# Performance work log

Hardware: AMD Instinct MI355X
Metric: run time of the kernel (lower is better)

Reference implementation:

```python
import jax, jax.numpy as jnp
import numpy as np

B = 1024          # batch
H = 512           # hidden_dim
T = 256           # seq_len
CD = 2            # coord_dim
LAT = 64 + 64 + 128  # total latent dim


def setup_inputs() -> dict:
    key = jax.random.key(0)
    ks = jax.random.split(key, 20)
    s = 0.05  # weight init scale
    rn = lambda k, shp: (jax.random.normal(k, shp, dtype=jnp.float32) * s)
    return {
        "z_primitive": jax.random.normal(ks[0], (B, 64), dtype=jnp.float32),
        "z_skill": jax.random.normal(ks[1], (B, 64), dtype=jnp.float32),
        "z_style": jax.random.normal(ks[2], (B, 128), dtype=jnp.float32),
        "W_proj": rn(ks[3], (2 * H, LAT)),
        "b_proj": jnp.zeros((2 * H,), jnp.float32),
        "Wih1": rn(ks[4], (4 * H, CD)),
        "Whh1": rn(ks[5], (4 * H, H)),
        "bih1": jnp.zeros((4 * H,), jnp.float32),
        "bhh1": jnp.zeros((4 * H,), jnp.float32),
        "Wih2": rn(ks[6], (4 * H, H)),
        "Whh2": rn(ks[7], (4 * H, H)),
        "bih2": jnp.zeros((4 * H,), jnp.float32),
        "bhh2": jnp.zeros((4 * H,), jnp.float32),
        "Wo1": rn(ks[8], (H // 2, H)),
        "bo1": jnp.zeros((H // 2,), jnp.float32),
        "Wo2": rn(ks[9], (CD, H // 2)),
        "bo2": jnp.zeros((CD,), jnp.float32),
    }


def _lstm_cell(x, h, c, Wih, Whh, bih, bhh):
    # PyTorch gate order: i, f, g, o
    gates = x @ Wih.T + h @ Whh.T + (bih + bhh)
    i, f, g, o = jnp.split(gates, 4, axis=1)
    c_new = jax.nn.sigmoid(f) * c + jax.nn.sigmoid(i) * jnp.tanh(g)
    h_new = jax.nn.sigmoid(o) * jnp.tanh(c_new)
    return h_new, c_new


def reference(z_primitive, z_skill, z_style, W_proj, b_proj,
              Wih1, Whh1, bih1, bhh1, Wih2, Whh2, bih2, bhh2,
              Wo1, bo1, Wo2, bo2):
    z = jnp.concatenate([z_primitive, z_skill, z_style], axis=1)  # [B, LAT]
    init = z @ W_proj.T + b_proj                                  # [B, 2H]
    h0 = init[:, :H]
    c0 = init[:, H:]
    x0 = jnp.zeros((z.shape[0], CD), init.dtype)

    def step(carry, _):
        x, h1, c1, h2, c2 = carry
        h1, c1 = _lstm_cell(x, h1, c1, Wih1, Whh1, bih1, bhh1)
        h2, c2 = _lstm_cell(h1, h2, c2, Wih2, Whh2, bih2, bhh2)
        # output MLP (Dropout inactive in eval)
        y = jax.nn.relu(h2 @ Wo1.T + bo1) @ Wo2.T + bo2  # [B, CD]
        return (y, h1, c1, h2, c2), y

    # h0/c0 repeated across both LSTM layers (repeat(2,1,1) in torch)
    _, ys = jax.lax.scan(step, (x0, h0, c0, h0, c0), None, length=T)
    return jnp.transpose(ys, (1, 0, 2))  # [B, T, CD]
```

## Files before the change

### kernel.cpp

```cpp
#include <hip/hip_runtime.h>
#include <math.h>

#define NB 1024
#define NH 512
#define NT 256
#define NCD 2

typedef unsigned short u16;
typedef __bf16 bf16x8 __attribute__((ext_vector_type(8)));
typedef float  f32x4  __attribute__((ext_vector_type(4)));

#define MFMA_BF16 __builtin_amdgcn_mfma_f32_16x16x32_bf16

__device__ __forceinline__ float sigf(float x) { return 1.0f / (1.0f + expf(-x)); }
__device__ __forceinline__ float b2f(u16 u) {
    union { unsigned i; float f; } v; v.i = ((unsigned)u) << 16; return v.f;
}
__device__ __forceinline__ u16 f2b(float f) {
    union { float f; unsigned i; } v; v.f = f;
    unsigned r = v.i + 0x7fffu + ((v.i >> 16) & 1u);
    return (u16)(r >> 16);
}

__device__ __forceinline__ void async_cp16(const void* gptr, void* lptr) {
    __builtin_amdgcn_global_load_lds(
        (const __attribute__((address_space(1))) unsigned int*)gptr,
        (__attribute__((address_space(3))) unsigned int*)lptr,
        16, 0, 0);
}

__global__ __launch_bounds__(256) void convert3(
    const float* __restrict__ a, const float* __restrict__ b,
    const float* __restrict__ c,
    u16* __restrict__ oa, u16* __restrict__ ob, u16* __restrict__ oc)
{
    const int i = blockIdx.x * 256 + threadIdx.x;
    oa[i] = f2b(a[i]); ob[i] = f2b(b[i]); oc[i] = f2b(c[i]);
}

__global__ __launch_bounds__(256) void convw1(
    const float* __restrict__ a, u16* __restrict__ o)
{
    const int i = blockIdx.x * 256 + threadIdx.x;
    o[i] = f2b(a[i]);
}

__global__ __launch_bounds__(256) void bsum_k(
    const float* __restrict__ bi1, const float* __restrict__ bh1,
    const float* __restrict__ bi2, const float* __restrict__ bh2,
    float* __restrict__ o1, float* __restrict__ o2)
{
    const int i = blockIdx.x * 256 + threadIdx.x;
    o1[i] = bi1[i] + bh1[i];
    o2[i] = bi2[i] + bh2[i];
}

__global__ __launch_bounds__(256) void init_kernel(
    const float* __restrict__ zp, const float* __restrict__ zs,
    const float* __restrict__ zst, const float* __restrict__ Wp,
    const float* __restrict__ bp,
    u16* __restrict__ h1, float* __restrict__ c1,
    u16* __restrict__ h2, float* __restrict__ c2)
{
    __shared__ float z[4][256];
    const int tid = threadIdx.x;
    const int b0  = blockIdx.x * 4;
    for (int i = tid; i < 4 * 256; i += 256) {
        const int bb = i >> 8, k = i & 255;
        float v;
        if (k < 64)       v = zp [(b0 + bb) * 64  + k];
        else if (k < 128) v = zs [(b0 + bb) * 64  + (k - 64)];
        else              v = zst[(b0 + bb) * 128 + (k - 128)];
        z[bb][k] = v;
    }
    __syncthreads();
    for (int rt = 0; rt < 4; ++rt) {
        const int r = rt * 256 + tid;
        const float bias = bp[r];
        float a0 = bias, a1 = bias, a2 = bias, a3 = bias;
        for (int k = 0; k < 256; ++k) {
            const float w = Wp[r * 256 + k];
            a0 += z[0][k] * w; a1 += z[1][k] * w;
            a2 += z[2][k] * w; a3 += z[3][k] * w;
        }
        const float acc[4] = {a0, a1, a2, a3};
        for (int bb = 0; bb < 4; ++bb) {
            const int b = b0 + bb;
            if (r < NH) {
                h1[b * NH + r] = f2b(acc[bb]);
                h2[b * NH + r] = f2b(acc[bb]);
            } else {
                c1[b * NH + r - NH] = acc[bb];
                c2[b * NH + r - NH] = acc[bb];
            }
        }
    }
}

__global__ __launch_bounds__(512, 4) void fused_out_lstm1(
    const u16* __restrict__ h2prev,
    const u16* __restrict__ A0,
    const u16* __restrict__ W0,
    const float* __restrict__ bsum,
    const float* __restrict__ Wx,
    const u16* __restrict__ W1b,
    const float* __restrict__ bo1, const float* __restrict__ Wo2,
    const float* __restrict__ bo2, float* __restrict__ outp,
    float* __restrict__ c, u16* __restrict__ hnext,
    const int t, const int do_lstm)
{
    __shared__ __align__(16) char smem[61440];
    float* eg  = (float*)smem;
    float* red = (float*)(smem + 36864);

    const int tid  = threadIdx.x;
    const int lane = tid & 63;
    const int wv   = tid >> 6;
    const int g    = wv & 3;
    const int mh   = wv >> 2;
    const int l15  = lane & 15;
    const int q    = lane >> 4;
    const int bx   = blockIdx.x;
    const int ut   = (bx & 7) * 2 + ((bx >> 3) & 1);
    const int grp  = bx >> 4;
    const int b0   = grp * 32;
    const int u0   = ut * 32;

    int goffW0, goffW1, goffA = 0, goffO[4];
    {
        const int c0 = (wv * 2) * 64 + lane;
        const int w0r = c0 >> 3;
        goffW0 = ((w0r >> 5) * NH + u0 + (w0r & 31)) * NH + (((c0 & 7) ^ (w0r & 7)) * 8);
        const int c1i = (wv * 2 + 1) * 64 + lane;
        const int w1r = c1i >> 3;
        goffW1 = ((w1r >> 5) * NH + u0 + (w1r & 31)) * NH + (((c1i & 7) ^ (w1r & 7)) * 8);
        if (wv < 4) {
            const int ca = wv * 64 + lane;
            const int ar = ca >> 3;
            goffA = (b0 + ar) * NH + (((ca & 7) ^ (ar & 7)) * 8);
        }
#pragma unroll
        for (int i = 0; i < 4; ++i) {
            const int cidx = (wv * 4 + i) * 64 + lane;
            const int row  = cidx >> 3;
            const int kc   = (cidx & 7) ^ (row & 7);
            goffO[i] = row * NH + kc * 8;
        }
    }

    auto issue = [&](int m, int bi) {
        const int k0 = (m & 7) * 64;
        char* base = smem + bi * 20480;
        async_cp16((const void*)(W0 + goffW0 + k0),
                   (void*)(base + 4096 + (wv * 2) * 1024));
        async_cp16((const void*)(W0 + goffW1 + k0),
                   (void*)(base + 4096 + (wv * 2 + 1) * 1024));
        if (wv < 4)
            async_cp16((const void*)(A0 + goffA + k0),
                       (void*)(base + wv * 1024));
    };

    const int u_e  = tid & 31;
    const int bq_e = tid >> 5;
    const int ug_e = u0 + u_e;
    float bs[4], wx0[4], wx1[4], cpre[2];
#pragma unroll
    for (int g4 = 0; g4 < 4; ++g4) bs[g4] = bsum[g4 * NH + ug_e];
#pragma unroll
    for (int g4 = 0; g4 < 4; ++g4) {
        wx0[g4] = Wx[(g4 * NH + ug_e) * 2 + 0];
        wx1[g4] = Wx[(g4 * NH + ug_e) * 2 + 1];
    }
    cpre[0] = c[(size_t)(b0 + bq_e * 2 + 0) * NH + ug_e];
    cpre[1] = c[(size_t)(b0 + bq_e * 2 + 1) * NH + ug_e];

    if (do_lstm) issue(0, 2);

    float r_x[4] = {0.f, 0.f, 0.f, 0.f};

    if (h2prev) {
        f32x4 acc_o[2][2];
#pragma unroll
        for (int mi = 0; mi < 2; ++mi)
#pragma unroll
            for (int ni = 0; ni < 2; ++ni)
                acc_o[mi][ni] = (f32x4){0.f, 0.f, 0.f, 0.f};

        for (int kk = 0; kk < 8; ++kk) {
            __syncthreads();
            const int k0 = kk * 64;
#pragma unroll
            for (int i = 0; i < 4; ++i)
                async_cp16((const void*)(W1b + goffO[i] + k0),
                           (void*)(smem + ((wv * 4 + i) << 10)));
            if (wv < 4)
                async_cp16((const void*)(h2prev + goffA + k0),
                           (void*)(smem + 32768 + (wv << 10)));
            asm volatile("s_waitcnt vmcnt(0)" ::: "memory");
            __builtin_amdgcn_s_barrier();
#pragma unroll
            for (int kh = 0; kh < 2; ++kh) {
                bf16x8 bfr[2], av[2];
#pragma unroll
                for (int ni = 0; ni < 2; ++ni) {
                    const int wrow = wv * 32 + ni * 16 + l15;
                    const int j = (kh * 4 + q) ^ (wrow & 7);
                    bfr[ni] = *(const bf16x8*)(smem + wrow * 128 + j * 16);
                }
#pragma unroll
                for (int mi = 0; mi < 2; ++mi) {
                    const int row = mi * 16 + l15;
                    const int j = (kh * 4 + q) ^ (row & 7);
                    av[mi] = *(const bf16x8*)(smem + 32768 + row * 128 + j * 16);
                }
#pragma unroll
                for (int mi = 0; mi < 2; ++mi)
#pragma unroll
                    for (int ni = 0; ni < 2; ++ni)
                        acc_o[mi][ni] = MFMA_BF16(av[mi], bfr[ni], acc_o[mi][ni], 0, 0, 0);
            }
        }
        float bo1n[2], w20[2], w21[2];
#pragma unroll
        for (int ni = 0; ni < 2; ++ni) {
            const int n = wv * 32 + ni * 16 + l15;
            bo1n[ni] = bo1[n]; w20[ni] = Wo2[n]; w21[ni] = Wo2[256 + n];
        }
        float pa[2][4], pb[2][4];
#pragma unroll
        for (int mi = 0; mi < 2; ++mi)
#pragma unroll
            for (int r = 0; r < 4; ++r) {
                const float s0 = fmaxf(acc_o[mi][0][r] + bo1n[0], 0.f);
                const float s1 = fmaxf(acc_o[mi][1][r] + bo1n[1], 0.f);
                pa[mi][r] = s0 * w20[0] + s1 * w20[1];
                pb[mi][r] = s0 * w21[0] + s1 * w21[1];
            }
#pragma unroll
        for (int off = 1; off < 16; off <<= 1)
#pragma unroll
            for (int mi = 0; mi < 2; ++mi)
#pragma unroll
                for (int r = 0; r < 4; ++r) {
                    pa[mi][r] += __shfl_xor(pa[mi][r], off, 64);
                    pb[mi][r] += __shfl_xor(pb[mi][r], off, 64);
                }
        if (l15 == 0) {
#pragma unroll
            for (int mi = 0; mi < 2; ++mi)
#pragma unroll
                for (int r = 0; r < 4; ++r) {
                    const int m = mi * 16 + q * 4 + r;
                    red[m * 16 + wv * 2 + 0] = pa[mi][r];
                    red[m * 16 + wv * 2 + 1] = pb[mi][r];
                }
        }
        __syncthreads();
        if (ut == 0 && tid < 64) {
            const int bl = tid >> 1, cc = tid & 1;
            float y = bo2[cc];
#pragma unroll
            for (int w8 = 0; w8 < 8; ++w8) y += red[bl * 16 + w8 * 2 + cc];
            outp[(size_t)(b0 + bl) * (NT * NCD) + (t - 1) * NCD + cc] = y;
        }
        if (do_lstm) {
            const int bq = tid >> 5;
#pragma unroll
            for (int jj = 0; jj < 2; ++jj)
#pragma unroll
                for (int cc = 0; cc < 2; ++cc) {
                    float y = bo2[cc];
#pragma unroll
                    for (int w8 = 0; w8 < 8; ++w8)
                        y += red[(bq * 2 + jj) * 16 + w8 * 2 + cc];
                    r_x[jj * 2 + cc] = y;
                }
        }
        __syncthreads();
    }
    if (!do_lstm) return;

    f32x4 acc[2];
    acc[0] = (f32x4){0.f, 0.f, 0.f, 0.f};
    acc[1] = (f32x4){0.f, 0.f, 0.f, 0.f};
    const int M = 8;
    issue(1, 0);
    int ci = 2;
    for (int m = 0; m < M; ++m) {
        if (m + 1 < M) {
            if (wv < 4) asm volatile("s_waitcnt vmcnt(3)" ::: "memory");
            else        asm volatile("s_waitcnt vmcnt(2)" ::: "memory");
        } else {
            asm volatile("s_waitcnt vmcnt(0)" ::: "memory");
        }
        __builtin_amdgcn_s_barrier();
        if (m + 2 < M) {
            int bi = ci + 2; if (bi >= 3) bi -= 3;
            issue(m + 2, bi);
        }
        const char* bA = smem + ci * 20480;
        const char* bW = bA + 4096;
#pragma unroll
        for (int khi = 0; khi < 2; ++khi) {
            bf16x8 bfr[2];
#pragma unroll
            for (int ni = 0; ni < 2; ++ni) {
                const int wrow = g * 32 + ni * 16 + l15;
                const int j = (khi * 4 + q) ^ (wrow & 7);
                bfr[ni] = *(const bf16x8*)(bW + wrow * 128 + j * 16);
            }
            const int row = mh * 16 + l15;
            const int j = (khi * 4 + q) ^ (row & 7);
            const bf16x8 av = *(const bf16x8*)(bA + row * 128 + j * 16);
            acc[0] = MFMA_BF16(av, bfr[0], acc[0], 0, 0, 0);
            acc[1] = MFMA_BF16(av, bfr[1], acc[1], 0, 0, 0);
        }
        ++ci; if (ci == 3) ci = 0;
    }

    __syncthreads();
#pragma unroll
    for (int ni = 0; ni < 2; ++ni)
#pragma unroll
        for (int r = 0; r < 4; ++r)
            eg[(g * 32 + mh * 16 + q * 4 + r) * 33 + ni * 16 + l15] = acc[ni][r];
    __syncthreads();

#pragma unroll
    for (int jj = 0; jj < 2; ++jj) {
        const int bl = bq_e * 2 + jj;
        const int b  = b0 + bl;
        float gv[4];
#pragma unroll
        for (int g4 = 0; g4 < 4; ++g4) gv[g4] = eg[(g4 * 32 + bl) * 33 + u_e] + bs[g4];
        const float x0 = r_x[jj * 2 + 0];
        const float x1 = r_x[jj * 2 + 1];
#pragma unroll
        for (int g4 = 0; g4 < 4; ++g4) gv[g4] += x0 * wx0[g4] + x1 * wx1[g4];
        const float iv = sigf(gv[0]);
        const float fv = sigf(gv[1]);
        const float gg = tanhf(gv[2]);
        const float ov = sigf(gv[3]);
        const size_t idx = (size_t)b * NH + ug_e;
        const float cn = fv * cpre[jj] + iv * gg;
        c[idx] = cn;
        hnext[idx] = f2b(ov * tanhf(cn));
    }
}

__global__ __launch_bounds__(512, 4) void lstm_mfma32(
    const u16* __restrict__ A0, const u16* __restrict__ W0,
    const u16* __restrict__ A1, const u16* __restrict__ W1,
    const float* __restrict__ bsum,
    float* __restrict__ c, u16* __restrict__ hnext,
    const int npass)
{
    __shared__ __align__(16) char smem[61440];
    float* eg = (float*)smem;

    const int tid  = threadIdx.x;
    const int lane = tid & 63;
    const int wv   = tid >> 6;
    const int g    = wv & 3;
    const int mh   = wv >> 2;
    const int l15  = lane & 15;
    const int q    = lane >> 4;
    const int bx   = blockIdx.x;
    const int ut   = (bx & 7) * 2 + ((bx >> 3) & 1);
    const int grp  = bx >> 4;
    const int b0   = grp * 32;
    const int u0   = ut * 32;

    int goffW0, goffW1, goffA = 0;
    {
        const int c0 = (wv * 2) * 64 + lane;
        const int w0r = c0 >> 3;
        goffW0 = ((w0r >> 5) * NH + u0 + (w0r & 31)) * NH + (((c0 & 7) ^ (w0r & 7)) * 8);
        const int c1i = (wv * 2 + 1) * 64 + lane;
        const int w1r = c1i >> 3;
        goffW1 = ((w1r >> 5) * NH + u0 + (w1r & 31)) * NH + (((c1i & 7) ^ (w1r & 7)) * 8);
        if (wv < 4) {
            const int ca = wv * 64 + lane;
            const int ar = ca >> 3;
            goffA = (b0 + ar) * NH + (((ca & 7) ^ (ar & 7)) * 8);
        }
    }

    const int u_e  = tid & 31;
    const int bq_e = tid >> 5;
    const int ug_e = u0 + u_e;
    float bs[4], cpre[2];
#pragma unroll
    for (int g4 = 0; g4 < 4; ++g4) bs[g4] = bsum[g4 * NH + ug_e];
    cpre[0] = c[(size_t)(b0 + bq_e * 2 + 0) * NH + ug_e];
    cpre[1] = c[(size_t)(b0 + bq_e * 2 + 1) * NH + ug_e];

    f32x4 acc[2];
    acc[0] = (f32x4){0.f, 0.f, 0.f, 0.f};
    acc[1] = (f32x4){0.f, 0.f, 0.f, 0.f};

    const int M = npass * 8;

    auto issue = [&](int m, int bi) {
        const u16* __restrict__ Ap = (m < 8) ? A0 : A1;
        const u16* __restrict__ Wp = (m < 8) ? W0 : W1;
        const int k0 = (m & 7) * 64;
        char* base = smem + bi * 20480;
        async_cp16((const void*)(Wp + goffW0 + k0),
                   (void*)(base + 4096 + (wv * 2) * 1024));
        async_cp16((const void*)(Wp + goffW1 + k0),
                   (void*)(base + 4096 + (wv * 2 + 1) * 1024));
        if (wv < 4)
            async_cp16((const void*)(Ap + goffA + k0),
                       (void*)(base + wv * 1024));
    };

    issue(0, 0);
    if (M > 1) issue(1, 1);
    int ci = 0;
    for (int m = 0; m < M; ++m) {
        if (m + 1 < M) {
            if (wv < 4) asm volatile("s_waitcnt vmcnt(3)" ::: "memory");
            else        asm volatile("s_waitcnt vmcnt(2)" ::: "memory");
        } else {
            asm volatile("s_waitcnt vmcnt(0)" ::: "memory");
        }
        __builtin_amdgcn_s_barrier();
        if (m + 2 < M) {
            int bi = ci + 2; if (bi >= 3) bi -= 3;
            issue(m + 2, bi);
        }
        const char* bA = smem + ci * 20480;
        const char* bW = bA + 4096;
#pragma unroll
        for (int khi = 0; khi < 2; ++khi) {
            bf16x8 bfr[2];
#pragma unroll
            for (int ni = 0; ni < 2; ++ni) {
                const int wrow = g * 32 + ni * 16 + l15;
                const int j = (khi * 4 + q) ^ (wrow & 7);
                bfr[ni] = *(const bf16x8*)(bW + wrow * 128 + j * 16);
            }
            const int row = mh * 16 + l15;
            const int j = (khi * 4 + q) ^ (row & 7);
            const bf16x8 av = *(const bf16x8*)(bA + row * 128 + j * 16);
            acc[0] = MFMA_BF16(av, bfr[0], acc[0], 0, 0, 0);
            acc[1] = MFMA_BF16(av, bfr[1], acc[1], 0, 0, 0);
        }
        ++ci; if (ci == 3) ci = 0;
    }

    __syncthreads();
#pragma unroll
    for (int ni = 0; ni < 2; ++ni)
#pragma unroll
        for (int r = 0; r < 4; ++r)
            eg[(g * 32 + mh * 16 + q * 4 + r) * 33 + ni * 16 + l15] = acc[ni][r];
    __syncthreads();

#pragma unroll
    for (int jj = 0; jj < 2; ++jj) {
        const int bl = bq_e * 2 + jj;
        const int b  = b0 + bl;
        float gv[4];
#pragma unroll
        for (int g4 = 0; g4 < 4; ++g4) gv[g4] = eg[(g4 * 32 + bl) * 33 + u_e] + bs[g4];
        const float iv = sigf(gv[0]);
        const float fv = sigf(gv[1]);
        const float gg = tanhf(gv[2]);
        const float ov = sigf(gv[3]);
        const size_t idx = (size_t)b * NH + ug_e;
        const float cn = fv * cpre[jj] + iv * gg;
        c[idx] = cn;
        hnext[idx] = f2b(ov * tanhf(cn));
    }
}

extern "C" void kernel_launch(void* const* d_in, const int* in_sizes, int n_in,
                              void* d_out, int out_size, void* d_ws, size_t ws_size,
                              hipStream_t stream)
{
    const float* zp   = (const float*)d_in[0];
    const float* zsk  = (const float*)d_in[1];
    const float* zst  = (const float*)d_in[2];
    const float* Wp   = (const float*)d_in[3];
    const float* bp   = (const float*)d_in[4];
    const float* Wih1 = (const float*)d_in[5];
    const float* Whh1 = (const float*)d_in[6];
    const float* bih1 = (const float*)d_in[7];
    const float* bhh1 = (const float*)d_in[8];
    const float* Wih2 = (const float*)d_in[9];
    const float* Whh2 = (const float*)d_in[10];
    const float* bih2 = (const float*)d_in[11];
    const float* bhh2 = (const float*)d_in[12];
    const float* Wo1  = (const float*)d_in[13];
    const float* bo1  = (const float*)d_in[14];
    const float* Wo2  = (const float*)d_in[15];
    const float* bo2  = (const float*)d_in[16];

    const size_t BH = (size_t)NB * NH;
    u16*   h1a   = (u16*)d_ws;
    u16*   h1b   = h1a + BH;
    u16*   h2a   = h1b + BH;
    u16*   h2b   = h2a + BH;
    float* c1    = (float*)(h2b + BH);
    float* c2    = c1 + BH;
    float* bs1   = c2 + BH;
    float* bs2   = bs1 + 2048;
    u16*   Wo1b  = (u16*)(bs2 + 2048);
    u16*   Whh1b = Wo1b + 131072;
    u16*   Wih2b = Whh1b + 1048576;
    u16*   Whh2b = Wih2b + 1048576;

    convert3<<<(2048 * 512) / 256, 256, 0, stream>>>(Whh1, Wih2, Whh2, Whh1b, Wih2b, Whh2b);
    convw1<<<(256 * 512) / 256, 256, 0, stream>>>(Wo1, Wo1b);
    bsum_k<<<2048 / 256, 256, 0, stream>>>(bih1, bhh1, bih2, bhh2, bs1, bs2);
    init_kernel<<<NB / 4, 256, 0, stream>>>(zp, zsk, zst, Wp, bp, h1a, c1, h2a, c2);

    u16* h1c = h1a; u16* h1n = h1b;
    u16* h2c = h2a; u16* h2n = h2b;
    float* outp = (float*)d_out;
    for (int t = 0; t < NT; ++t) {
        fused_out_lstm1<<<512, 512, 0, stream>>>(
            (t == 0) ? (const u16*)0 : h2c, h1c, Whh1b, bs1, Wih1,
            Wo1b, bo1, Wo2, bo2, outp, c1, h1n, t, 1);
        lstm_mfma32<<<512, 512, 0, stream>>>(h1n, Wih2b, h2c, Whh2b,
                                             bs2, c2, h2n, 2);
        u16* tmp = h1c; h1c = h1n; h1n = tmp;
        tmp = h2c; h2c = h2n; h2n = tmp;
    }
    fused_out_lstm1<<<512, 512, 0, stream>>>(
        h2c, h1c, Whh1b, bs1, Wih1,
        Wo1b, bo1, Wo2, bo2, outp, c1, h1n, NT, 0);
}
```

Before: 7.473 ms.

## Stage activations fully in LDS and stream weights directly from global into registers

The layer-2 LSTM kernel no longer runs a triple-buffered LDS pipeline over K chunks for both weights and activations. It now loads the whole 32x512 h1 and h2 activation tiles into LDS once, then each wave reads its weight fragments straight from global memory into MFMA operand registers while iterating over K. The wave-to-tile mapping also changes so that each wave owns one gate and a 16-unit slice across both batch halves. This removes per-chunk barriers and LDS staging of weights, but the weight loads are now uncoalesced per-lane global reads with no software prefetch, and LDS use grows to 64 KB, which may limit occupancy.

```diff
diff --git a/kernel.cpp b/kernel.cpp
--- a/kernel.cpp
+++ b/kernel.cpp
@@ -348,21 +348,20 @@
     }
 }
 
-__global__ __launch_bounds__(512, 4) void lstm_mfma32(
-    const u16* __restrict__ A0, const u16* __restrict__ W0,
-    const u16* __restrict__ A1, const u16* __restrict__ W1,
+__global__ __launch_bounds__(512, 4) void lstm2_kernel(
+    const u16* __restrict__ A0,
+    const u16* __restrict__ W0,
+    const u16* __restrict__ A1,
+    const u16* __restrict__ W1,
     const float* __restrict__ bsum,
-    float* __restrict__ c, u16* __restrict__ hnext,
-    const int npass)
-{
-    __shared__ __align__(16) char smem[61440];
+    float* __restrict__ c, u16* __restrict__ hnext)
+{
+    __shared__ __align__(16) char smem[65536];
     float* eg = (float*)smem;
 
     const int tid  = threadIdx.x;
     const int lane = tid & 63;
     const int wv   = tid >> 6;
-    const int g    = wv & 3;
-    const int mh   = wv >> 2;
     const int l15  = lane & 15;
     const int q    = lane >> 4;
     const int bx   = blockIdx.x;
@@ -370,21 +369,25 @@
     const int grp  = bx >> 4;
     const int b0   = grp * 32;
     const int u0   = ut * 32;
-
-    int goffW0, goffW1, goffA = 0;
-    {
-        const int c0 = (wv * 2) * 64 + lane;
-        const int w0r = c0 >> 3;
-        goffW0 = ((w0r >> 5) * NH + u0 + (w0r & 31)) * NH + (((c0 & 7) ^ (w0r & 7)) * 8);
-        const int c1i = (wv * 2 + 1) * 64 + lane;
-        const int w1r = c1i >> 3;
-        goffW1 = ((w1r >> 5) * NH + u0 + (w1r & 31)) * NH + (((c1i & 7) ^ (w1r & 7)) * 8);
-        if (wv < 4) {
-            const int ca = wv * 64 + lane;
-            const int ar = ca >> 3;
-            goffA = (b0 + ar) * NH + (((ca & 7) ^ (ar & 7)) * 8);
-        }
-    }
+    const int gw   = wv >> 1;
+    const int uh   = wv & 1;
+
+    int goffT[4];
+#pragma unroll
+    for (int i = 0; i < 4; ++i) {
+        const int cidx = (wv * 4 + i) * 64 + lane;
+        const int row  = (cidx >> 3) & 31;
+        const int slot = cidx & 7;
+        goffT[i] = (b0 + row) * NH + (cidx >> 8) * 64 + ((slot ^ (row & 7)) * 8);
+    }
+#pragma unroll
+    for (int i = 0; i < 4; ++i)
+        async_cp16((const void*)(A0 + goffT[i]),
+                   (void*)(smem + ((wv * 4 + i) << 10)));
+#pragma unroll
+    for (int i = 0; i < 4; ++i)
+        async_cp16((const void*)(A1 + goffT[i]),
+                   (void*)(smem + 32768 + ((wv * 4 + i) << 10)));
 
     const int u_e  = tid & 31;
     const int bq_e = tid >> 5;
@@ -395,67 +398,49 @@
     cpre[0] = c[(size_t)(b0 + bq_e * 2 + 0) * NH + ug_e];
     cpre[1] = c[(size_t)(b0 + bq_e * 2 + 1) * NH + ug_e];
 
+    const size_t wrow = (size_t)(gw * NH + u0 + uh * 16 + l15) * NH + q * 8;
+    const u16* pW0 = W0 + wrow;
+    const u16* pW1 = W1 + wrow;
+
+    asm volatile("s_waitcnt vmcnt(0)" ::: "memory");
+    __syncthreads();
+
     f32x4 acc[2];
     acc[0] = (f32x4){0.f, 0.f, 0.f, 0.f};
     acc[1] = (f32x4){0.f, 0.f, 0.f, 0.f};
-
-    const int M = npass * 8;
-
-    auto issue = [&](int m, int bi) {
-        const u16* __restrict__ Ap = (m < 8) ? A0 : A1;
-        const u16* __restrict__ Wp = (m < 8) ? W0 : W1;
-        const int k0 = (m & 7) * 64;
-        char* base = smem + bi * 20480;
-        async_cp16((const void*)(Wp + goffW0 + k0),
-                   (void*)(base + 4096 + (wv * 2) * 1024));
-        async_cp16((const void*)(Wp + goffW1 + k0),
-                   (void*)(base + 4096 + (wv * 2 + 1) * 1024));
-        if (wv < 4)
-            async_cp16((const void*)(Ap + goffA + k0),
-                       (void*)(base + wv * 1024));
-    };
-
-    issue(0, 0);
-    if (M > 1) issue(1, 1);
-    int ci = 0;
-    for (int m = 0; m < M; ++m) {
-        if (m + 1 < M) {
-            if (wv < 4) asm volatile("s_waitcnt vmcnt(3)" ::: "memory");
-            else        asm volatile("s_waitcnt vmcnt(2)" ::: "memory");
-        } else {
-            asm volatile("s_waitcnt vmcnt(0)" ::: "memory");
-        }
-        __builtin_amdgcn_s_barrier();
-        if (m + 2 < M) {
-            int bi = ci + 2; if (bi >= 3) bi -= 3;
-            issue(m + 2, bi);
-        }
-        const char* bA = smem + ci * 20480;
-        const char* bW = bA + 4096;
-#pragma unroll
-        for (int khi = 0; khi < 2; ++khi) {
-            bf16x8 bfr[2];
-#pragma unroll
-            for (int ni = 0; ni < 2; ++ni) {
-                const int wrow = g * 32 + ni * 16 + l15;
-                const int j = (khi * 4 + q) ^ (wrow & 7);
-                bfr[ni] = *(const bf16x8*)(bW + wrow * 128 + j * 16);
-            }
-            const int row = mh * 16 + l15;
-            const int j = (khi * 4 + q) ^ (row & 7);
-            const bf16x8 av = *(const bf16x8*)(bA + row * 128 + j * 16);
-            acc[0] = MFMA_BF16(av, bfr[0], acc[0], 0, 0, 0);
-            acc[1] = MFMA_BF16(av, bfr[1], acc[1], 0, 0, 0);
-        }
-        ++ci; if (ci == 3) ci = 0;
+#pragma unroll
+    for (int s = 0; s < 16; ++s) {
+        const bf16x8 bfr = *(const bf16x8*)(pW0 + s * 32);
+        bf16x8 av[2];
+#pragma unroll
+        for (int mi = 0; mi < 2; ++mi) {
+            const int row = mi * 16 + l15;
+            const int j = ((s & 1) * 4 + q) ^ (row & 7);
+            av[mi] = *(const bf16x8*)(smem + (s >> 1) * 4096 + row * 128 + j * 16);
+        }
+        acc[0] = MFMA_BF16(av[0], bfr, acc[0], 0, 0, 0);
+        acc[1] = MFMA_BF16(av[1], bfr, acc[1], 0, 0, 0);
+    }
+#pragma unroll
+    for (int s = 0; s < 16; ++s) {
+        const bf16x8 bfr = *(const bf16x8*)(pW1 + s * 32);
+        bf16x8 av[2];
+#pragma unroll
+        for (int mi = 0; mi < 2; ++mi) {
+            const int row = mi * 16 + l15;
+            const int j = ((s & 1) * 4 + q) ^ (row & 7);
+            av[mi] = *(const bf16x8*)(smem + 32768 + (s >> 1) * 4096 + row * 128 + j * 16);
+        }
+        acc[0] = MFMA_BF16(av[0], bfr, acc[0], 0, 0, 0);
+        acc[1] = MFMA_BF16(av[1], bfr, acc[1], 0, 0, 0);
     }
 
     __syncthreads();
 #pragma unroll
-    for (int ni = 0; ni < 2; ++ni)
+    for (int mi = 0; mi < 2; ++mi)
 #pragma unroll
         for (int r = 0; r < 4; ++r)
-            eg[(g * 32 + mh * 16 + q * 4 + r) * 33 + ni * 16 + l15] = acc[ni][r];
+            eg[(gw * 32 + mi * 16 + q * 4 + r) * 33 + uh * 16 + l15] = acc[mi][r];
     __syncthreads();
 
 #pragma unroll
@@ -524,8 +509,8 @@
         fused_out_lstm1<<<512, 512, 0, stream>>>(
             (t == 0) ? (const u16*)0 : h2c, h1c, Whh1b, bs1, Wih1,
             Wo1b, bo1, Wo2, bo2, outp, c1, h1n, t, 1);
-        lstm_mfma32<<<512, 512, 0, stream>>>(h1n, Wih2b, h2c, Whh2b,
-                                             bs2, c2, h2n, 2);
+        lstm2_kernel<<<512, 512, 0, stream>>>(h1n, Wih2b, h2c, Whh2b,
+                                              bs2, c2, h2n);
         u16* tmp = h1c; h1c = h1n; h1n = tmp;
         tmp = h2c; h2c = h2n; h2n = tmp;
     }
```

Result: slower. 9.586 ms (+28.3%).
